# Performance work log

Measured on AMD Instinct MI355X. Metric: run time of the kernel, lower is better.

Reference implementation:

```python
import jax, jax.numpy as jnp
import numpy as np

H = 64          # HIDDEN_DIM
V = 64          # VOCAB_SIZE
THR = 0.4       # ENERGY_THRESHOLD
LN_EPS = 1e-5
NORM_EPS = 1e-12


def _layer_norm(x, g, b):
    mu = jnp.mean(x, axis=-1, keepdims=True)
    var = jnp.var(x, axis=-1, keepdims=True)
    return (x - mu) * jax.lax.rsqrt(var + LN_EPS) * g + b


def setup_inputs() -> dict:
    key = jax.random.key(0)
    ks = jax.random.split(key, 12)
    B, L = 256, 2048
    s = 0.05
    return {
        "x": jax.random.randint(ks[0], (B, L), 0, V),
        "embed": jax.random.normal(ks[1], (V, H), jnp.float32) * s,
        "w1": jax.random.normal(ks[2], (H, 2 * H), jnp.float32) * s,
        "b1": jnp.zeros((2 * H,), jnp.float32),
        "w2": jax.random.normal(ks[3], (2 * H, H), jnp.float32) * s,
        "b2": jnp.zeros((H,), jnp.float32),
        "ln_g": jnp.ones((H,), jnp.float32),
        "ln_b": jnp.zeros((H,), jnp.float32),
        "wk": jax.random.normal(ks[4], (H, H), jnp.float32) * s,
        "wv": jax.random.normal(ks[5], (H, H), jnp.float32) * s,
        "wq": jax.random.normal(ks[6], (H, H), jnp.float32) * s,
        "wo": jax.random.normal(ks[7], (H, V), jnp.float32) * s,
        "bo": jnp.zeros((V,), jnp.float32),
    }


def reference(x, embed, w1, b1, w2, b2, ln_g, ln_b, wk, wv, wq, wo, bo):
    # Encoder: embed -> FFN -> residual -> LayerNorm
    h = embed[x]                                        # [B, L, H]
    ff = jax.nn.relu(h @ w1 + b1) @ w2 + b2
    h = _layer_norm(h + ff, ln_g, ln_b)                 # [B, L, H]

    B = h.shape[0]
    # Precompute all k (L2-normalized) and v projections, then scan over time.
    k = h @ wk                                          # [B, L, H]
    k = k / jnp.maximum(jnp.linalg.norm(k, axis=-1, keepdims=True), NORM_EPS)
    v = h @ wv                                          # [B, L, H]

    def step(M, kv):
        k_t, v_t = kv                                   # each [B, H]
        pred = jnp.einsum('bij,bj->bi', M, k_t)         # [B, H]
        delta = v_t - pred
        gate = (jnp.linalg.norm(delta, axis=-1, keepdims=True)
                > THR * jnp.linalg.norm(v_t, axis=-1, keepdims=True)).astype(M.dtype)
        M = M + gate[:, :, None] * jnp.einsum('bi,bj->bij', delta, k_t)
        return M, None

    M0 = jnp.zeros((B, H, H), h.dtype)
    M, _ = jax.lax.scan(step, M0,
                        (jnp.swapaxes(k, 0, 1), jnp.swapaxes(v, 0, 1)))

    q = h[:, -1, :] @ wq                                # [B, H]
    read = jax.nn.relu(jnp.einsum('bij,bj->bi', M, q))  # [B, H]
    return read @ wo + bo                               # [B, V]
```

## Files before the change

### kernel.cpp

```cpp
#include <hip/hip_runtime.h>
#include <hip/hip_bf16.h>

#define HD   64
#define SEQ  2048
#define NB   256
#define TWOH 128
#define NCH  32

typedef float v4f __attribute__((ext_vector_type(4)));

template <int CTRL>
__device__ __forceinline__ float dpp_add(float x) {
    int y = __builtin_amdgcn_update_dpp(0, __builtin_bit_cast(int, x),
                                        CTRL, 0xF, 0xF, true);
    return x + __builtin_bit_cast(float, y);
}

__device__ __forceinline__ float wave_total(float x) {
    x = dpp_add<0x111>(x);
    x = dpp_add<0x112>(x);
    x = dpp_add<0x114>(x);
    x = dpp_add<0x118>(x);
    x = dpp_add<0x142>(x);
    x = dpp_add<0x143>(x);
    return __builtin_bit_cast(float,
        __builtin_amdgcn_readlane(__builtin_bit_cast(int, x), 63));
}

__device__ __forceinline__ float bcastf(float v, int l) {
    return __builtin_bit_cast(float,
        __builtin_amdgcn_readlane(__builtin_bit_cast(int, v), l));
}

__device__ __forceinline__ float hsum4(v4f a) {
    return (a.x + a.y) + (a.z + a.w);
}

__device__ __forceinline__ bool detect_bf16(const void* embed, int lane) {
    const unsigned short* u = (const unsigned short*)embed;
    int bad = 0;
    for (int i = 2 * lane; i < 4096; i += 128) {
        float v = __uint_as_float(((unsigned int)u[i]) << 16);
        if (!(fabsf(v) < 1e4f)) bad = 1;
    }
    return !__any(bad);
}

template <bool BF>
__device__ __forceinline__ float ldf(const void* p, int i) {
    if (BF) return __bfloat162float(((const __hip_bfloat16*)p)[i]);
    return ((const float*)p)[i];
}

template <bool BF>
__device__ void encode16(int wid, int lane, const void* embed, const void* w1,
                         const void* b1, const void* w2, const void* b2,
                         const void* ln_g, const void* ln_b, const void* wk,
                         const void* wvp, const void* wq,
                         float* __restrict__ k_lds, float* __restrict__ v_lds,
                         float* __restrict__ q_lds, float* __restrict__ thr2_lds,
                         float* __restrict__ shh, float* __restrict__ shu) {
    #pragma unroll 1
    for (int it = 0; it < 16; ++it) {
        const int t = wid * 16 + it;
        float h = ldf<BF>(embed, t * HD + lane);
        shh[lane] = h;
        asm volatile("s_waitcnt lgkmcnt(0)" ::: "memory");

        float a0 = 0.f, a1 = 0.f, a2 = 0.f, a3 = 0.f;
        #pragma unroll 16
        for (int j = 0; j < HD; j += 2) {
            float h0 = shh[j], h1 = shh[j + 1];
            a0 = fmaf(h0, ldf<BF>(w1, j * TWOH + lane), a0);
            a1 = fmaf(h0, ldf<BF>(w1, j * TWOH + lane + HD), a1);
            a2 = fmaf(h1, ldf<BF>(w1, (j + 1) * TWOH + lane), a2);
            a3 = fmaf(h1, ldf<BF>(w1, (j + 1) * TWOH + lane + HD), a3);
        }
        shu[lane]      = fmaxf(a0 + a2 + ldf<BF>(b1, lane), 0.f);
        shu[lane + HD] = fmaxf(a1 + a3 + ldf<BF>(b1, lane + HD), 0.f);
        asm volatile("s_waitcnt lgkmcnt(0)" ::: "memory");

        float f0 = 0.f, f1 = 0.f, f2 = 0.f, f3 = 0.f;
        #pragma unroll 16
        for (int e = 0; e < TWOH; e += 4) {
            f0 = fmaf(shu[e + 0], ldf<BF>(w2, (e + 0) * HD + lane), f0);
            f1 = fmaf(shu[e + 1], ldf<BF>(w2, (e + 1) * HD + lane), f1);
            f2 = fmaf(shu[e + 2], ldf<BF>(w2, (e + 2) * HD + lane), f2);
            f3 = fmaf(shu[e + 3], ldf<BF>(w2, (e + 3) * HD + lane), f3);
        }
        float y = h + (f0 + f1) + (f2 + f3) + ldf<BF>(b2, lane);

        float mu  = wave_total(y) * 0.015625f;
        float dvv = y - mu;
        float var = wave_total(dvv * dvv) * 0.015625f;
        float hn  = fmaf(dvv * (1.f / sqrtf(var + 1e-5f)), ldf<BF>(ln_g, lane),
                         ldf<BF>(ln_b, lane));

        shh[lane] = hn;
        asm volatile("s_waitcnt lgkmcnt(0)" ::: "memory");

        float k0 = 0.f, k1 = 0.f, v0 = 0.f, v1 = 0.f, q0 = 0.f, q1 = 0.f;
        #pragma unroll 16
        for (int j = 0; j < HD; j += 2) {
            float h0 = shh[j], h1 = shh[j + 1];
            k0 = fmaf(h0, ldf<BF>(wk, j * HD + lane), k0);
            v0 = fmaf(h0, ldf<BF>(wvp, j * HD + lane), v0);
            q0 = fmaf(h0, ldf<BF>(wq, j * HD + lane), q0);
            k1 = fmaf(h1, ldf<BF>(wk, (j + 1) * HD + lane), k1);
            v1 = fmaf(h1, ldf<BF>(wvp, (j + 1) * HD + lane), v1);
            q1 = fmaf(h1, ldf<BF>(wq, (j + 1) * HD + lane), q1);
        }
        float k = k0 + k1, v = v0 + v1, q = q0 + q1;
        float nk = sqrtf(wave_total(k * k));
        k /= fmaxf(nk, 1e-12f);
        float nv2 = wave_total(v * v);

        k_lds[t * HD + lane] = k;
        v_lds[t * HD + lane] = v;
        q_lds[t * HD + lane] = q;
        if (lane == 0) thr2_lds[t] = 0.16f * nv2;
    }
}

__global__ __launch_bounds__(256, 1) void fused_kernel(
    const int* __restrict__ x, const void* embed, const void* w1,
    const void* b1, const void* w2, const void* b2, const void* ln_g,
    const void* ln_b, const void* wk, const void* wvp, const void* wq,
    const void* wo, const void* bo, void* __restrict__ out) {
    const int b = blockIdx.x, tid = threadIdx.x;
    const int wid = tid >> 6, lane = tid & 63;
    __shared__ __align__(16) float k_lds[4096];
    __shared__ __align__(16) float g_lds[4096];
    __shared__ __align__(16) float v_lds[4096];
    __shared__ __align__(16) float q_lds[4096];
    __shared__ int   tok_lds[SEQ];
    __shared__ float thr2_lds[64];
    __shared__ float pbuf[2][4][64];
    __shared__ __align__(16) float rd_lds[64];
    __shared__ float sh_h[4][HD];
    __shared__ float sh_u[4][TWOH];

    const int* xr = x + b * SEQ;
    #pragma unroll
    for (int c = 0; c < 8; ++c) tok_lds[c * 256 + tid] = xr[c * 256 + tid];

    const bool bf = detect_bf16(embed, lane);
    if (bf)
        encode16<true>(wid, lane, embed, w1, b1, w2, b2, ln_g, ln_b, wk, wvp,
                       wq, k_lds, v_lds, q_lds, thr2_lds, sh_h[wid], sh_u[wid]);
    else
        encode16<false>(wid, lane, embed, w1, b1, w2, b2, ln_g, ln_b, wk, wvp,
                        wq, k_lds, v_lds, q_lds, thr2_lds, sh_h[wid], sh_u[wid]);
    __syncthreads();

    const float thr2 = thr2_lds[lane];

    v4f kreg[16];
    #pragma unroll
    for (int i = 0; i < 16; ++i)
        kreg[i] = *(const v4f*)&k_lds[lane * HD + i * 4];

    const int tl = tok_lds[SEQ - 1];
    v4f cacc = {0.f, 0.f, 0.f, 0.f};
    #pragma unroll
    for (int i = 0; i < 16; ++i) {
        const float* qp = &q_lds[tl * HD + i * 4];
        v4f qv = {qp[0], qp[1], qp[2], qp[3]};
        cacc = __builtin_elementwise_fma(qv, kreg[i], cacc);
    }
    const float cq = hsum4(cacc);

    #pragma unroll 1
    for (int t0 = 0; t0 < 16; ++t0) {
        const int t = wid * 16 + t0;
        const float* kt = &k_lds[t * HD];
        v4f a = {0.f, 0.f, 0.f, 0.f};
        #pragma unroll
        for (int i = 0; i < 16; ++i) {
            const v4f kv = *(const v4f*)&kt[i * 4];
            a = __builtin_elementwise_fma(kv, kreg[i], a);
        }
        g_lds[t * HD + lane] = hsum4(a);
    }

    v4f dv[4], R[4];
    v4f acc = {0.f, 0.f, 0.f, 0.f};
    #pragma unroll
    for (int i = 0; i < 4; ++i) {
        dv[i] = *(const v4f*)&v_lds[lane * HD + wid * 16 + i * 4];
        R[i]  = (v4f){0.f, 0.f, 0.f, 0.f};
        acc   = __builtin_elementwise_fma(dv[i], dv[i], acc);
    }
    pbuf[0][wid][lane] = hsum4(acc);
    int pp = 1;
    __syncthreads();
    float nd2 = ((pbuf[0][0][lane] + pbuf[0][1][lane]) +
                 (pbuf[0][2][lane] + pbuf[0][3][lane]));
    unsigned long long fireset = __ballot(nd2 > thr2);

    int chunk = tok_lds[lane];
    #pragma unroll 1
    for (int c = 0; c < NCH; ++c) {
        int nxt = 0;
        if (c + 1 < NCH) nxt = tok_lds[(c + 1) * 64 + lane];
        unsigned long long pend = __ballot((int)((fireset >> chunk) & 1ull));
        while (pend) {
            const int s = __builtin_ctzll(pend);
            const int t = __builtin_amdgcn_readlane(chunk, s);
            const float g   = g_lds[t * HD + lane];
            const float cqt = bcastf(cq, t);
            const v4f gs  = {-g, -g, -g, -g};
            const v4f cqs = {cqt, cqt, cqt, cqt};
            v4f q4 = {0.f, 0.f, 0.f, 0.f};
            #pragma unroll
            for (int i = 0; i < 4; ++i) {
                v4f sve;
                sve.x = bcastf(dv[i].x, t);
                sve.y = bcastf(dv[i].y, t);
                sve.z = bcastf(dv[i].z, t);
                sve.w = bcastf(dv[i].w, t);
                dv[i] = __builtin_elementwise_fma(gs, sve, dv[i]);
                R[i]  = __builtin_elementwise_fma(cqs, sve, R[i]);
                q4    = __builtin_elementwise_fma(dv[i], dv[i], q4);
            }
            pbuf[pp][wid][lane] = hsum4(q4);
            __syncthreads();
            nd2 = ((pbuf[pp][0][lane] + pbuf[pp][1][lane]) +
                   (pbuf[pp][2][lane] + pbuf[pp][3][lane]));
            pp ^= 1;
            fireset = __ballot(nd2 > thr2);
            const unsigned long long above =
                (s >= 63) ? 0ull : (~0ull << (s + 1));
            pend = __ballot((int)((fireset >> chunk) & 1ull)) & above;
        }
        chunk = nxt;
    }

    if (lane == 0) {
        #pragma unroll
        for (int i = 0; i < 4; ++i) {
            v4f r = R[i];
            r.x = fmaxf(r.x, 0.f); r.y = fmaxf(r.y, 0.f);
            r.z = fmaxf(r.z, 0.f); r.w = fmaxf(r.w, 0.f);
            *(v4f*)&rd_lds[wid * 16 + i * 4] = r;
        }
    }
    __syncthreads();

    if (wid == 0) {
        if (bf) {
            float acc2 = __bfloat162float(((const __hip_bfloat16*)bo)[lane]);
            #pragma unroll 8
            for (int j = 0; j < HD; ++j)
                acc2 = fmaf(rd_lds[j],
                    __bfloat162float(((const __hip_bfloat16*)wo)[j * HD + lane]),
                    acc2);
            ((__hip_bfloat16*)out)[b * HD + lane] = __float2bfloat16(acc2);
        } else {
            float acc2 = ((const float*)bo)[lane];
            #pragma unroll 8
            for (int j = 0; j < HD; ++j)
                acc2 = fmaf(rd_lds[j], ((const float*)wo)[j * HD + lane], acc2);
            ((float*)out)[b * HD + lane] = acc2;
        }
    }
}

extern "C" void kernel_launch(void* const* d_in, const int* in_sizes, int n_in,
                              void* d_out, int out_size, void* d_ws, size_t ws_size,
                              hipStream_t stream) {
    const int* x      = (const int*)d_in[0];
    const void* embed = d_in[1];
    const void* w1    = d_in[2];
    const void* b1    = d_in[3];
    const void* w2    = d_in[4];
    const void* b2    = d_in[5];
    const void* ln_g  = d_in[6];
    const void* ln_b  = d_in[7];
    const void* wk    = d_in[8];
    const void* wvp   = d_in[9];
    const void* wq    = d_in[10];
    const void* wo    = d_in[11];
    const void* bo    = d_in[12];

    fused_kernel<<<NB, 256, 0, stream>>>(x, embed, w1, b1, w2, b2, ln_g, ln_b,
                                         wk, wvp, wq, wo, bo, d_out);
}
```

Before: 319.1 us.

## Batch encoder over 16 vocab rows per wave to reuse weight loads

The per-token encoder loop is restructured so each wave processes its 16 vocabulary rows together. Each weight element is loaded once and applied to all 16 rows held in registers and LDS, where before the weights were reloaded for every row. The q projection is now computed only for the last token's row instead of all 64, and LDS buffers are reshuffled (q_lds dropped, g buffer reused as a scratch buffer). This raises register pressure from the 16-wide accumulator arrays and adds LDS traffic for the staged rows.

```diff
diff --git a/kernel.cpp b/kernel.cpp
--- a/kernel.cpp
+++ b/kernel.cpp
@@ -52,73 +52,160 @@
     return ((const float*)p)[i];
 }
 
+#define LGKM_BARRIER() asm volatile("s_waitcnt lgkmcnt(0)" ::: "memory")
+
 template <bool BF>
-__device__ void encode16(int wid, int lane, const void* embed, const void* w1,
-                         const void* b1, const void* w2, const void* b2,
-                         const void* ln_g, const void* ln_b, const void* wk,
-                         const void* wvp, const void* wq,
-                         float* __restrict__ k_lds, float* __restrict__ v_lds,
-                         float* __restrict__ q_lds, float* __restrict__ thr2_lds,
-                         float* __restrict__ shh, float* __restrict__ shu) {
-    #pragma unroll 1
+__device__ void encode_stream(int wid, int lane, int tl, const void* embed,
+                              const void* w1, const void* b1, const void* w2,
+                              const void* b2, const void* ln_g, const void* ln_b,
+                              const void* wk, const void* wvp, const void* wq,
+                              float* __restrict__ k_lds, float* __restrict__ v_lds,
+                              float* __restrict__ thr2_lds,
+                              float* __restrict__ qrow,
+                              float* __restrict__ hb,
+                              float* __restrict__ ub) {
+    const int tbase = wid * 16;
+    float h[16];
+    #pragma unroll
     for (int it = 0; it < 16; ++it) {
-        const int t = wid * 16 + it;
-        float h = ldf<BF>(embed, t * HD + lane);
-        shh[lane] = h;
-        asm volatile("s_waitcnt lgkmcnt(0)" ::: "memory");
-
-        float a0 = 0.f, a1 = 0.f, a2 = 0.f, a3 = 0.f;
-        #pragma unroll 16
-        for (int j = 0; j < HD; j += 2) {
-            float h0 = shh[j], h1 = shh[j + 1];
-            a0 = fmaf(h0, ldf<BF>(w1, j * TWOH + lane), a0);
-            a1 = fmaf(h0, ldf<BF>(w1, j * TWOH + lane + HD), a1);
-            a2 = fmaf(h1, ldf<BF>(w1, (j + 1) * TWOH + lane), a2);
-            a3 = fmaf(h1, ldf<BF>(w1, (j + 1) * TWOH + lane + HD), a3);
-        }
-        shu[lane]      = fmaxf(a0 + a2 + ldf<BF>(b1, lane), 0.f);
-        shu[lane + HD] = fmaxf(a1 + a3 + ldf<BF>(b1, lane + HD), 0.f);
-        asm volatile("s_waitcnt lgkmcnt(0)" ::: "memory");
-
-        float f0 = 0.f, f1 = 0.f, f2 = 0.f, f3 = 0.f;
-        #pragma unroll 16
-        for (int e = 0; e < TWOH; e += 4) {
-            f0 = fmaf(shu[e + 0], ldf<BF>(w2, (e + 0) * HD + lane), f0);
-            f1 = fmaf(shu[e + 1], ldf<BF>(w2, (e + 1) * HD + lane), f1);
-            f2 = fmaf(shu[e + 2], ldf<BF>(w2, (e + 2) * HD + lane), f2);
-            f3 = fmaf(shu[e + 3], ldf<BF>(w2, (e + 3) * HD + lane), f3);
-        }
-        float y = h + (f0 + f1) + (f2 + f3) + ldf<BF>(b2, lane);
-
+        h[it] = ldf<BF>(embed, (tbase + it) * HD + lane);
+        hb[it * HD + lane] = h[it];
+    }
+    LGKM_BARRIER();
+
+    float u0[16], u1[16];
+    #pragma unroll
+    for (int it = 0; it < 16; ++it) { u0[it] = 0.f; u1[it] = 0.f; }
+    #pragma unroll 1
+    for (int j4 = 0; j4 < 16; ++j4) {
+        const int j = j4 * 4;
+        float wa0 = ldf<BF>(w1, (j + 0) * TWOH + lane);
+        float wb0 = ldf<BF>(w1, (j + 0) * TWOH + lane + HD);
+        float wa1 = ldf<BF>(w1, (j + 1) * TWOH + lane);
+        float wb1 = ldf<BF>(w1, (j + 1) * TWOH + lane + HD);
+        float wa2 = ldf<BF>(w1, (j + 2) * TWOH + lane);
+        float wb2 = ldf<BF>(w1, (j + 2) * TWOH + lane + HD);
+        float wa3 = ldf<BF>(w1, (j + 3) * TWOH + lane);
+        float wb3 = ldf<BF>(w1, (j + 3) * TWOH + lane + HD);
+        #pragma unroll
+        for (int it = 0; it < 16; ++it) {
+            const v4f hj = *(const v4f*)&hb[it * HD + j];
+            u0[it] = fmaf(hj.x, wa0, u0[it]); u1[it] = fmaf(hj.x, wb0, u1[it]);
+            u0[it] = fmaf(hj.y, wa1, u0[it]); u1[it] = fmaf(hj.y, wb1, u1[it]);
+            u0[it] = fmaf(hj.z, wa2, u0[it]); u1[it] = fmaf(hj.z, wb2, u1[it]);
+            u0[it] = fmaf(hj.w, wa3, u0[it]); u1[it] = fmaf(hj.w, wb3, u1[it]);
+        }
+    }
+    const float bb0 = ldf<BF>(b1, lane), bb1 = ldf<BF>(b1, lane + HD);
+    #pragma unroll
+    for (int it = 0; it < 16; ++it) {
+        u0[it] = fmaxf(u0[it] + bb0, 0.f);
+        u1[it] = fmaxf(u1[it] + bb1, 0.f);
+    }
+
+    float f[16];
+    #pragma unroll
+    for (int it = 0; it < 16; ++it) f[it] = 0.f;
+    LGKM_BARRIER();
+    #pragma unroll
+    for (int it = 0; it < 16; ++it) ub[it * HD + lane] = u0[it];
+    LGKM_BARRIER();
+    #pragma unroll 1
+    for (int e4 = 0; e4 < 16; ++e4) {
+        const int e = e4 * 4;
+        float w0 = ldf<BF>(w2, (e + 0) * HD + lane);
+        float w1v = ldf<BF>(w2, (e + 1) * HD + lane);
+        float w2v = ldf<BF>(w2, (e + 2) * HD + lane);
+        float w3 = ldf<BF>(w2, (e + 3) * HD + lane);
+        #pragma unroll
+        for (int it = 0; it < 16; ++it) {
+            const v4f ue = *(const v4f*)&ub[it * HD + e];
+            f[it] = fmaf(ue.x, w0, f[it]);
+            f[it] = fmaf(ue.y, w1v, f[it]);
+            f[it] = fmaf(ue.z, w2v, f[it]);
+            f[it] = fmaf(ue.w, w3, f[it]);
+        }
+    }
+    LGKM_BARRIER();
+    #pragma unroll
+    for (int it = 0; it < 16; ++it) ub[it * HD + lane] = u1[it];
+    LGKM_BARRIER();
+    #pragma unroll 1
+    for (int e4 = 0; e4 < 16; ++e4) {
+        const int e = e4 * 4;
+        float w0 = ldf<BF>(w2, (HD + e + 0) * HD + lane);
+        float w1v = ldf<BF>(w2, (HD + e + 1) * HD + lane);
+        float w2v = ldf<BF>(w2, (HD + e + 2) * HD + lane);
+        float w3 = ldf<BF>(w2, (HD + e + 3) * HD + lane);
+        #pragma unroll
+        for (int it = 0; it < 16; ++it) {
+            const v4f ue = *(const v4f*)&ub[it * HD + e];
+            f[it] = fmaf(ue.x, w0, f[it]);
+            f[it] = fmaf(ue.y, w1v, f[it]);
+            f[it] = fmaf(ue.z, w2v, f[it]);
+            f[it] = fmaf(ue.w, w3, f[it]);
+        }
+    }
+    const float b2v = ldf<BF>(b2, lane);
+    const float lg = ldf<BF>(ln_g, lane), lb = ldf<BF>(ln_b, lane);
+
+    LGKM_BARRIER();
+    #pragma unroll 1
+    for (int it = 0; it < 16; ++it) {
+        float y = h[it] + f[it] + b2v;
         float mu  = wave_total(y) * 0.015625f;
         float dvv = y - mu;
         float var = wave_total(dvv * dvv) * 0.015625f;
-        float hn  = fmaf(dvv * (1.f / sqrtf(var + 1e-5f)), ldf<BF>(ln_g, lane),
-                         ldf<BF>(ln_b, lane));
-
-        shh[lane] = hn;
-        asm volatile("s_waitcnt lgkmcnt(0)" ::: "memory");
-
-        float k0 = 0.f, k1 = 0.f, v0 = 0.f, v1 = 0.f, q0 = 0.f, q1 = 0.f;
-        #pragma unroll 16
-        for (int j = 0; j < HD; j += 2) {
-            float h0 = shh[j], h1 = shh[j + 1];
-            k0 = fmaf(h0, ldf<BF>(wk, j * HD + lane), k0);
-            v0 = fmaf(h0, ldf<BF>(wvp, j * HD + lane), v0);
-            q0 = fmaf(h0, ldf<BF>(wq, j * HD + lane), q0);
-            k1 = fmaf(h1, ldf<BF>(wk, (j + 1) * HD + lane), k1);
-            v1 = fmaf(h1, ldf<BF>(wvp, (j + 1) * HD + lane), v1);
-            q1 = fmaf(h1, ldf<BF>(wq, (j + 1) * HD + lane), q1);
-        }
-        float k = k0 + k1, v = v0 + v1, q = q0 + q1;
-        float nk = sqrtf(wave_total(k * k));
-        k /= fmaxf(nk, 1e-12f);
-        float nv2 = wave_total(v * v);
-
-        k_lds[t * HD + lane] = k;
-        v_lds[t * HD + lane] = v;
-        q_lds[t * HD + lane] = q;
+        float hn  = fmaf(dvv * (1.f / sqrtf(var + 1e-5f)), lg, lb);
+        hb[it * HD + lane] = hn;
+    }
+    LGKM_BARRIER();
+
+    float k[16], v[16];
+    #pragma unroll
+    for (int it = 0; it < 16; ++it) { k[it] = 0.f; v[it] = 0.f; }
+    #pragma unroll 1
+    for (int j4 = 0; j4 < 16; ++j4) {
+        const int j = j4 * 4;
+        float ka = ldf<BF>(wk, (j + 0) * HD + lane);
+        float kb = ldf<BF>(wk, (j + 1) * HD + lane);
+        float kc = ldf<BF>(wk, (j + 2) * HD + lane);
+        float kd = ldf<BF>(wk, (j + 3) * HD + lane);
+        float va = ldf<BF>(wvp, (j + 0) * HD + lane);
+        float vb = ldf<BF>(wvp, (j + 1) * HD + lane);
+        float vc = ldf<BF>(wvp, (j + 2) * HD + lane);
+        float vd = ldf<BF>(wvp, (j + 3) * HD + lane);
+        #pragma unroll
+        for (int it = 0; it < 16; ++it) {
+            const v4f hj = *(const v4f*)&hb[it * HD + j];
+            k[it] = fmaf(hj.x, ka, k[it]); v[it] = fmaf(hj.x, va, v[it]);
+            k[it] = fmaf(hj.y, kb, k[it]); v[it] = fmaf(hj.y, vb, v[it]);
+            k[it] = fmaf(hj.z, kc, k[it]); v[it] = fmaf(hj.z, vc, v[it]);
+            k[it] = fmaf(hj.w, kd, k[it]); v[it] = fmaf(hj.w, vd, v[it]);
+        }
+    }
+    #pragma unroll 1
+    for (int it = 0; it < 16; ++it) {
+        const int t = tbase + it;
+        float nk = sqrtf(wave_total(k[it] * k[it]));
+        float kn = k[it] / fmaxf(nk, 1e-12f);
+        float nv2 = wave_total(v[it] * v[it]);
+        k_lds[t * HD + lane] = kn;
+        v_lds[t * HD + lane] = v[it];
         if (lane == 0) thr2_lds[t] = 0.16f * nv2;
+    }
+    if (tl >= tbase && tl < tbase + 16) {
+        float q = 0.f;
+        const int it = tl - tbase;
+        #pragma unroll
+        for (int j4 = 0; j4 < 16; ++j4) {
+            const v4f hj = *(const v4f*)&hb[it * HD + j4 * 4];
+            q = fmaf(hj.x, ldf<BF>(wq, (j4 * 4 + 0) * HD + lane), q);
+            q = fmaf(hj.y, ldf<BF>(wq, (j4 * 4 + 1) * HD + lane), q);
+            q = fmaf(hj.z, ldf<BF>(wq, (j4 * 4 + 2) * HD + lane), q);
+            q = fmaf(hj.w, ldf<BF>(wq, (j4 * 4 + 3) * HD + lane), q);
+        }
+        qrow[lane] = q;
     }
 }
 
@@ -130,27 +217,29 @@
     const int b = blockIdx.x, tid = threadIdx.x;
     const int wid = tid >> 6, lane = tid & 63;
     __shared__ __align__(16) float k_lds[4096];
-    __shared__ __align__(16) float g_lds[4096];
     __shared__ __align__(16) float v_lds[4096];
-    __shared__ __align__(16) float q_lds[4096];
+    __shared__ __align__(16) float gu_lds[4096];
+    __shared__ __align__(16) float hbuf[4096];
     __shared__ int   tok_lds[SEQ];
     __shared__ float thr2_lds[64];
+    __shared__ float qrow[64];
     __shared__ float pbuf[2][4][64];
     __shared__ __align__(16) float rd_lds[64];
-    __shared__ float sh_h[4][HD];
-    __shared__ float sh_u[4][TWOH];
 
     const int* xr = x + b * SEQ;
     #pragma unroll
     for (int c = 0; c < 8; ++c) tok_lds[c * 256 + tid] = xr[c * 256 + tid];
+    const int tl = xr[SEQ - 1];
 
     const bool bf = detect_bf16(embed, lane);
     if (bf)
-        encode16<true>(wid, lane, embed, w1, b1, w2, b2, ln_g, ln_b, wk, wvp,
-                       wq, k_lds, v_lds, q_lds, thr2_lds, sh_h[wid], sh_u[wid]);
+        encode_stream<true>(wid, lane, tl, embed, w1, b1, w2, b2, ln_g, ln_b,
+                            wk, wvp, wq, k_lds, v_lds, thr2_lds, qrow,
+                            &hbuf[wid * 1024], &gu_lds[wid * 1024]);
     else
-        encode16<false>(wid, lane, embed, w1, b1, w2, b2, ln_g, ln_b, wk, wvp,
-                        wq, k_lds, v_lds, q_lds, thr2_lds, sh_h[wid], sh_u[wid]);
+        encode_stream<false>(wid, lane, tl, embed, w1, b1, w2, b2, ln_g, ln_b,
+                             wk, wvp, wq, k_lds, v_lds, thr2_lds, qrow,
+                             &hbuf[wid * 1024], &gu_lds[wid * 1024]);
     __syncthreads();
 
     const float thr2 = thr2_lds[lane];
@@ -160,12 +249,10 @@
     for (int i = 0; i < 16; ++i)
         kreg[i] = *(const v4f*)&k_lds[lane * HD + i * 4];
 
-    const int tl = tok_lds[SEQ - 1];
     v4f cacc = {0.f, 0.f, 0.f, 0.f};
     #pragma unroll
     for (int i = 0; i < 16; ++i) {
-        const float* qp = &q_lds[tl * HD + i * 4];
-        v4f qv = {qp[0], qp[1], qp[2], qp[3]};
+        const v4f qv = *(const v4f*)&qrow[i * 4];
         cacc = __builtin_elementwise_fma(qv, kreg[i], cacc);
     }
     const float cq = hsum4(cacc);
@@ -180,7 +267,7 @@
             const v4f kv = *(const v4f*)&kt[i * 4];
             a = __builtin_elementwise_fma(kv, kreg[i], a);
         }
-        g_lds[t * HD + lane] = hsum4(a);
+        gu_lds[t * HD + lane] = hsum4(a);
     }
 
     v4f dv[4], R[4];
@@ -207,7 +294,7 @@
         while (pend) {
             const int s = __builtin_ctzll(pend);
             const int t = __builtin_amdgcn_readlane(chunk, s);
-            const float g   = g_lds[t * HD + lane];
+            const float g   = gu_lds[t * HD + lane];
             const float cqt = bcastf(cq, t);
             const v4f gs  = {-g, -g, -g, -g};
             const v4f cqs = {cqt, cqt, cqt, cqt};
```

New measurement: 283.5 us. 11.2% less time.

## Split per-token encoder across blocks via global workspace and grid sync

Applied to the files above, without the earlier changes.

Each block previously encoded all 64 vocabulary rows itself. Now blocks 0-63 each encode one vocab row into a global workspace, followed by a cooperative grid sync, and every block reads k/v/q/thresholds from that workspace. This removes redundant encoder work from every block at the cost of a cooperative launch, a grid-wide barrier and extra global memory reads.

```diff
diff --git a/kernel.cpp b/kernel.cpp
--- a/kernel.cpp
+++ b/kernel.cpp
@@ -1,5 +1,6 @@
 #include <hip/hip_runtime.h>
 #include <hip/hip_bf16.h>
+#include <hip/hip_cooperative_groups.h>
 
 #define HD   64
 #define SEQ  2048
@@ -8,6 +9,10 @@
 #define NCH  32
 
 typedef float v4f __attribute__((ext_vector_type(4)));
+
+#define WS_V    4096
+#define WS_Q    8192
+#define WS_THR  12288
 
 template <int CTRL>
 __device__ __forceinline__ float dpp_add(float x) {
@@ -52,123 +57,131 @@
     return ((const float*)p)[i];
 }
 
+#define LGKM_BARRIER() asm volatile("s_waitcnt lgkmcnt(0)" ::: "memory")
+
 template <bool BF>
-__device__ void encode16(int wid, int lane, const void* embed, const void* w1,
-                         const void* b1, const void* w2, const void* b2,
-                         const void* ln_g, const void* ln_b, const void* wk,
-                         const void* wvp, const void* wq,
-                         float* __restrict__ k_lds, float* __restrict__ v_lds,
-                         float* __restrict__ q_lds, float* __restrict__ thr2_lds,
-                         float* __restrict__ shh, float* __restrict__ shu) {
-    #pragma unroll 1
-    for (int it = 0; it < 16; ++it) {
-        const int t = wid * 16 + it;
-        float h = ldf<BF>(embed, t * HD + lane);
-        shh[lane] = h;
-        asm volatile("s_waitcnt lgkmcnt(0)" ::: "memory");
-
-        float a0 = 0.f, a1 = 0.f, a2 = 0.f, a3 = 0.f;
-        #pragma unroll 16
-        for (int j = 0; j < HD; j += 2) {
-            float h0 = shh[j], h1 = shh[j + 1];
-            a0 = fmaf(h0, ldf<BF>(w1, j * TWOH + lane), a0);
-            a1 = fmaf(h0, ldf<BF>(w1, j * TWOH + lane + HD), a1);
-            a2 = fmaf(h1, ldf<BF>(w1, (j + 1) * TWOH + lane), a2);
-            a3 = fmaf(h1, ldf<BF>(w1, (j + 1) * TWOH + lane + HD), a3);
-        }
-        shu[lane]      = fmaxf(a0 + a2 + ldf<BF>(b1, lane), 0.f);
-        shu[lane + HD] = fmaxf(a1 + a3 + ldf<BF>(b1, lane + HD), 0.f);
-        asm volatile("s_waitcnt lgkmcnt(0)" ::: "memory");
-
-        float f0 = 0.f, f1 = 0.f, f2 = 0.f, f3 = 0.f;
-        #pragma unroll 16
-        for (int e = 0; e < TWOH; e += 4) {
-            f0 = fmaf(shu[e + 0], ldf<BF>(w2, (e + 0) * HD + lane), f0);
-            f1 = fmaf(shu[e + 1], ldf<BF>(w2, (e + 1) * HD + lane), f1);
-            f2 = fmaf(shu[e + 2], ldf<BF>(w2, (e + 2) * HD + lane), f2);
-            f3 = fmaf(shu[e + 3], ldf<BF>(w2, (e + 3) * HD + lane), f3);
-        }
-        float y = h + (f0 + f1) + (f2 + f3) + ldf<BF>(b2, lane);
-
-        float mu  = wave_total(y) * 0.015625f;
-        float dvv = y - mu;
-        float var = wave_total(dvv * dvv) * 0.015625f;
-        float hn  = fmaf(dvv * (1.f / sqrtf(var + 1e-5f)), ldf<BF>(ln_g, lane),
-                         ldf<BF>(ln_b, lane));
-
-        shh[lane] = hn;
-        asm volatile("s_waitcnt lgkmcnt(0)" ::: "memory");
-
-        float k0 = 0.f, k1 = 0.f, v0 = 0.f, v1 = 0.f, q0 = 0.f, q1 = 0.f;
-        #pragma unroll 16
-        for (int j = 0; j < HD; j += 2) {
-            float h0 = shh[j], h1 = shh[j + 1];
-            k0 = fmaf(h0, ldf<BF>(wk, j * HD + lane), k0);
-            v0 = fmaf(h0, ldf<BF>(wvp, j * HD + lane), v0);
-            q0 = fmaf(h0, ldf<BF>(wq, j * HD + lane), q0);
-            k1 = fmaf(h1, ldf<BF>(wk, (j + 1) * HD + lane), k1);
-            v1 = fmaf(h1, ldf<BF>(wvp, (j + 1) * HD + lane), v1);
-            q1 = fmaf(h1, ldf<BF>(wq, (j + 1) * HD + lane), q1);
-        }
-        float k = k0 + k1, v = v0 + v1, q = q0 + q1;
-        float nk = sqrtf(wave_total(k * k));
-        k /= fmaxf(nk, 1e-12f);
-        float nv2 = wave_total(v * v);
-
-        k_lds[t * HD + lane] = k;
-        v_lds[t * HD + lane] = v;
-        q_lds[t * HD + lane] = q;
-        if (lane == 0) thr2_lds[t] = 0.16f * nv2;
-    }
+__device__ void encode1(int t, int lane, const void* embed, const void* w1,
+                        const void* b1, const void* w2, const void* b2,
+                        const void* ln_g, const void* ln_b, const void* wk,
+                        const void* wvp, const void* wq, float* __restrict__ ws,
+                        float* __restrict__ shh, float* __restrict__ shu) {
+    float h = ldf<BF>(embed, t * HD + lane);
+    shh[lane] = h;
+    LGKM_BARRIER();
+
+    float a0 = 0.f, a1 = 0.f, a2 = 0.f, a3 = 0.f;
+    #pragma unroll 16
+    for (int j = 0; j < HD; j += 2) {
+        float h0 = shh[j], h1 = shh[j + 1];
+        a0 = fmaf(h0, ldf<BF>(w1, j * TWOH + lane), a0);
+        a1 = fmaf(h0, ldf<BF>(w1, j * TWOH + lane + HD), a1);
+        a2 = fmaf(h1, ldf<BF>(w1, (j + 1) * TWOH + lane), a2);
+        a3 = fmaf(h1, ldf<BF>(w1, (j + 1) * TWOH + lane + HD), a3);
+    }
+    shu[lane]      = fmaxf(a0 + a2 + ldf<BF>(b1, lane), 0.f);
+    shu[lane + HD] = fmaxf(a1 + a3 + ldf<BF>(b1, lane + HD), 0.f);
+    LGKM_BARRIER();
+
+    float f0 = 0.f, f1 = 0.f, f2 = 0.f, f3 = 0.f;
+    #pragma unroll 16
+    for (int e = 0; e < TWOH; e += 4) {
+        f0 = fmaf(shu[e + 0], ldf<BF>(w2, (e + 0) * HD + lane), f0);
+        f1 = fmaf(shu[e + 1], ldf<BF>(w2, (e + 1) * HD + lane), f1);
+        f2 = fmaf(shu[e + 2], ldf<BF>(w2, (e + 2) * HD + lane), f2);
+        f3 = fmaf(shu[e + 3], ldf<BF>(w2, (e + 3) * HD + lane), f3);
+    }
+    float y = h + (f0 + f1) + (f2 + f3) + ldf<BF>(b2, lane);
+
+    float mu  = wave_total(y) * 0.015625f;
+    float dvv = y - mu;
+    float var = wave_total(dvv * dvv) * 0.015625f;
+    float hn  = fmaf(dvv * (1.f / sqrtf(var + 1e-5f)), ldf<BF>(ln_g, lane),
+                     ldf<BF>(ln_b, lane));
+
+    LGKM_BARRIER();
+    shh[lane] = hn;
+    LGKM_BARRIER();
+
+    float k0 = 0.f, k1 = 0.f, v0 = 0.f, v1 = 0.f, q0 = 0.f, q1 = 0.f;
+    #pragma unroll 16
+    for (int j = 0; j < HD; j += 2) {
+        float h0 = shh[j], h1 = shh[j + 1];
+        k0 = fmaf(h0, ldf<BF>(wk, j * HD + lane), k0);
+        v0 = fmaf(h0, ldf<BF>(wvp, j * HD + lane), v0);
+        q0 = fmaf(h0, ldf<BF>(wq, j * HD + lane), q0);
+        k1 = fmaf(h1, ldf<BF>(wk, (j + 1) * HD + lane), k1);
+        v1 = fmaf(h1, ldf<BF>(wvp, (j + 1) * HD + lane), v1);
+        q1 = fmaf(h1, ldf<BF>(wq, (j + 1) * HD + lane), q1);
+    }
+    float k = k0 + k1, v = v0 + v1, q = q0 + q1;
+    float nk = sqrtf(wave_total(k * k));
+    k /= fmaxf(nk, 1e-12f);
+    float nv2 = wave_total(v * v);
+
+    ws[t * HD + lane]        = k;
+    ws[WS_V + t * HD + lane] = v;
+    ws[WS_Q + t * HD + lane] = q;
+    if (lane == 0) ws[WS_THR + t] = 0.16f * nv2;
 }
 
 __global__ __launch_bounds__(256, 1) void fused_kernel(
     const int* __restrict__ x, const void* embed, const void* w1,
     const void* b1, const void* w2, const void* b2, const void* ln_g,
     const void* ln_b, const void* wk, const void* wvp, const void* wq,
-    const void* wo, const void* bo, void* __restrict__ out) {
+    const void* wo, const void* bo, float* __restrict__ ws,
+    void* __restrict__ out) {
     const int b = blockIdx.x, tid = threadIdx.x;
     const int wid = tid >> 6, lane = tid & 63;
     __shared__ __align__(16) float k_lds[4096];
     __shared__ __align__(16) float g_lds[4096];
-    __shared__ __align__(16) float v_lds[4096];
-    __shared__ __align__(16) float q_lds[4096];
     __shared__ int   tok_lds[SEQ];
-    __shared__ float thr2_lds[64];
     __shared__ float pbuf[2][4][64];
     __shared__ __align__(16) float rd_lds[64];
-    __shared__ float sh_h[4][HD];
-    __shared__ float sh_u[4][TWOH];
+    __shared__ float enc_h[HD];
+    __shared__ float enc_u[TWOH];
 
     const int* xr = x + b * SEQ;
     #pragma unroll
     for (int c = 0; c < 8; ++c) tok_lds[c * 256 + tid] = xr[c * 256 + tid];
+    const int tl = xr[SEQ - 1];
 
     const bool bf = detect_bf16(embed, lane);
-    if (bf)
-        encode16<true>(wid, lane, embed, w1, b1, w2, b2, ln_g, ln_b, wk, wvp,
-                       wq, k_lds, v_lds, q_lds, thr2_lds, sh_h[wid], sh_u[wid]);
-    else
-        encode16<false>(wid, lane, embed, w1, b1, w2, b2, ln_g, ln_b, wk, wvp,
-                        wq, k_lds, v_lds, q_lds, thr2_lds, sh_h[wid], sh_u[wid]);
-    __syncthreads();
-
-    const float thr2 = thr2_lds[lane];
+
+    if (b < 64 && wid == 0) {
+        if (bf)
+            encode1<true>(b, lane, embed, w1, b1, w2, b2, ln_g, ln_b,
+                          wk, wvp, wq, ws, enc_h, enc_u);
+        else
+            encode1<false>(b, lane, embed, w1, b1, w2, b2, ln_g, ln_b,
+                           wk, wvp, wq, ws, enc_h, enc_u);
+        __threadfence();
+    }
+    cooperative_groups::this_grid().sync();
+
+    #pragma unroll
+    for (int i = 0; i < 4; ++i) {
+        int o = i * 1024 + tid * 4;
+        *(float4*)&k_lds[o] = *(const float4*)&ws[o];
+    }
+    const float thr2 = ws[WS_THR + lane];
 
     v4f kreg[16];
-    #pragma unroll
-    for (int i = 0; i < 16; ++i)
-        kreg[i] = *(const v4f*)&k_lds[lane * HD + i * 4];
-
-    const int tl = tok_lds[SEQ - 1];
+    const float* krow = ws + lane * HD;
+    #pragma unroll
+    for (int i = 0; i < 16; ++i) {
+        float4 kv = *(const float4*)&krow[i * 4];
+        kreg[i] = (v4f){kv.x, kv.y, kv.z, kv.w};
+    }
+    const float* qrow = ws + WS_Q + tl * HD;
     v4f cacc = {0.f, 0.f, 0.f, 0.f};
     #pragma unroll
     for (int i = 0; i < 16; ++i) {
-        const float* qp = &q_lds[tl * HD + i * 4];
+        const float* qp = &qrow[i * 4];
         v4f qv = {qp[0], qp[1], qp[2], qp[3]};
         cacc = __builtin_elementwise_fma(qv, kreg[i], cacc);
     }
     const float cq = hsum4(cacc);
+    __syncthreads();
 
     #pragma unroll 1
     for (int t0 = 0; t0 < 16; ++t0) {
@@ -184,10 +197,12 @@
     }
 
     v4f dv[4], R[4];
+    const float* vr = ws + WS_V + lane * HD + wid * 16;
     v4f acc = {0.f, 0.f, 0.f, 0.f};
     #pragma unroll
     for (int i = 0; i < 4; ++i) {
-        dv[i] = *(const v4f*)&v_lds[lane * HD + wid * 16 + i * 4];
+        float4 vvv = *(const float4*)&vr[i * 4];
+        dv[i] = (v4f){vvv.x, vvv.y, vvv.z, vvv.w};
         R[i]  = (v4f){0.f, 0.f, 0.f, 0.f};
         acc   = __builtin_elementwise_fma(dv[i], dv[i], acc);
     }
@@ -282,7 +297,13 @@
     const void* wq    = d_in[10];
     const void* wo    = d_in[11];
     const void* bo    = d_in[12];
-
-    fused_kernel<<<NB, 256, 0, stream>>>(x, embed, w1, b1, w2, b2, ln_g, ln_b,
-                                         wk, wvp, wq, wo, bo, d_out);
-}
+    float* ws = (float*)d_ws;
+    void* outp = d_out;
+
+    void* kargs[] = {
+        (void*)&x, (void*)&embed, (void*)&w1, (void*)&b1, (void*)&w2,
+        (void*)&b2, (void*)&ln_g, (void*)&ln_b, (void*)&wk, (void*)&wvp,
+        (void*)&wq, (void*)&wo, (void*)&bo, (void*)&ws, (void*)&outp};
+    hipLaunchCooperativeKernel((const void*)fused_kernel, dim3(NB), dim3(256),
+                               kargs, 0, stream);
+}
```

Result: no change. 316.3 us (-0.9%).
